# Kernel optimization log

Measured on AMD Instinct MI355X. Metric: run time of the kernel, lower is better.

## Reference

```python
import jax, jax.numpy as jnp
import numpy as np

N, T, DIN, E, D, L, G = 50000, 1, 7, 800000, 64, 3, 64


def _lin(key, fi, fo):
    k1, k2 = jax.random.split(key)
    s = 1.0 / np.sqrt(fi)
    return (jax.random.uniform(k1, (fi, fo), jnp.float32, -s, s),
            jax.random.uniform(k2, (fo,), jnp.float32, -s, s))


def setup_inputs() -> dict:
    key = jax.random.key(0)
    ks = jax.random.split(key, 16)
    x = jax.random.normal(ks[0], (N, T, DIN), jnp.float32)
    edge_index = jax.random.randint(ks[1], (2, E), 0, N).astype(jnp.int64)
    edge_attr = jax.random.uniform(ks[2], (E, T), jnp.float32)
    batch = jnp.sort(jax.random.randint(ks[3], (N,), 0, G)).astype(jnp.int64)
    degree = jax.random.uniform(ks[4], (N,), jnp.float32)
    W_en, b_en = _lin(ks[5], DIN, D)
    W_ene, b_ene = _lin(ks[6], DIN + 1, D - 1)
    W_agg, b_agg = _lin(ks[7], D, D)
    Wm = []; bm = []; Wu = []; bu = []
    for l in range(L):
        w, b = _lin(jax.random.fold_in(ks[8], l), 2 * D, D); Wm.append(w); bm.append(b)
        w, b = _lin(jax.random.fold_in(ks[9], l), 2 * D, D); Wu.append(w); bu.append(b)
    Wm = jnp.stack(Wm); bm = jnp.stack(bm); Wu = jnp.stack(Wu); bu = jnp.stack(bu)
    W_g, b_g = _lin(ks[10], D, D)
    W_r, b_r = _lin(ks[11], 2 * D, 1)
    return dict(x=x, edge_index=edge_index, edge_attr=edge_attr, batch=batch,
                degree=degree, num_graphs=G,
                W_en=W_en, b_en=b_en, W_ene=W_ene, b_ene=b_ene,
                W_agg=W_agg, b_agg=b_agg, Wm=Wm, bm=bm, Wu=Wu, bu=bu,
                W_g=W_g, b_g=b_g, W_r=W_r, b_r=b_r)


def _scatter_mean(vals, idx, n):
    # vals: [M, T, F] -> [n, T, F]; empty segments -> 0 (count clamped to 1)
    s = jax.ops.segment_sum(vals, idx, num_segments=n)
    c = jax.ops.segment_sum(jnp.ones((vals.shape[0], 1, 1), vals.dtype), idx, num_segments=n)
    return s / jnp.maximum(c, 1.0)


def reference(x, edge_index, edge_attr, batch, degree, num_graphs,
              W_en, b_en, W_ene, b_ene, W_agg, b_agg,
              Wm, bm, Wu, bu, W_g, b_g, W_r, b_r):
    relu = jax.nn.relu
    col, row = edge_index[0], edge_index[1]
    n = x.shape[0]
    x_emb = relu(x @ W_en + b_en)                                   # [N,T,D]
    # node+edge embedding: gather source nodes, append edge_attr, mean over dst
    ne_in = jnp.concatenate([x[col], edge_attr[:, :, None]], axis=-1)  # [E,T,DIN+1]
    node_edge = _scatter_mean(ne_in, row, n)                        # [N,T,DIN+1]
    node_edge = relu(node_edge @ W_ene + b_ene)                     # [N,T,D-1]
    deg_max = jax.ops.segment_max(degree, batch, num_segments=num_graphs)
    degree_norm = deg_max[batch][:, None, None]                     # [N,1,1] -> broadcast over T
    degree_norm = jnp.broadcast_to(degree_norm, (n, node_edge.shape[1], 1))
    x_agg_emb = relu(jnp.concatenate([node_edge, degree_norm], axis=-1) @ W_agg + b_agg)
    for l in range(Wm.shape[0]):
        x_agg = _scatter_mean(edge_attr[:, :, None] * x_emb[col], row, n)   # [N,T,D]
        m = relu(jnp.concatenate([x_agg, x_agg_emb], axis=-1) @ Wm[l] + bm[l])
        x_emb = relu(jnp.concatenate([x_emb, m], axis=-1) @ Wu[l] + bu[l])
    g_agg = _scatter_mean(x_emb, batch, num_graphs)                 # [G,T,D]
    g_agg = g_agg @ W_g + b_g
    inp = jnp.concatenate([g_agg[batch], x_emb], axis=-1)           # [N,T,2D]
    q = relu(inp) @ W_r + b_r                                       # [N,T,1]
    return jnp.squeeze(q, axis=-1)                                  # [N,T]
```

## Files before the change

### kernel.cpp

```cpp
#include <hip/hip_runtime.h>

constexpr int NN  = 50000;
constexpr int EE  = 800000;
constexpr int GG  = 64;
constexpr int LL  = 3;

__device__ __forceinline__ float reluf(float x) { return x > 0.f ? x : 0.f; }

__global__ void k_count(const int* __restrict__ ei, int* __restrict__ cnt,
                        int* __restrict__ rel) {
    int e = blockIdx.x * blockDim.x + threadIdx.x;
    if (e >= EE) return;
    rel[e] = atomicAdd(&cnt[ei[EE + e]], 1);
}

__global__ void k_scan1(const int* __restrict__ cnt, int* __restrict__ off,
                        int* __restrict__ bsum,
                        const int* __restrict__ batch, const float* __restrict__ degree,
                        unsigned* __restrict__ degmax_u, int* __restrict__ g_cnt) {
    __shared__ int s[256];
    __shared__ unsigned smax[GG];
    __shared__ int scnt[GG];
    int t = threadIdx.x, blk = blockIdx.x;
    if (t < GG) { smax[t] = 0u; scnt[t] = 0; }
    int base = blk * 1024 + t * 4;
    int v[4], tot = 0;
#pragma unroll
    for (int j = 0; j < 4; j++) {
        int i = base + j;
        v[j] = (i < NN) ? cnt[i] : 0;
        tot += v[j];
    }
    s[t] = tot;
    __syncthreads();
    {
        int curb = -1; unsigned cur = 0u; int ccnt = 0;
#pragma unroll
        for (int j = 0; j < 4; j++) {
            int i = base + j;
            if (i < NN) {
                int b = batch[i];
                unsigned d = __float_as_uint(degree[i]);
                if (b != curb) {
                    if (curb >= 0) { atomicMax(&smax[curb], cur); atomicAdd(&scnt[curb], ccnt); }
                    curb = b; cur = d; ccnt = 1;
                } else {
                    if (d > cur) cur = d;
                    ccnt++;
                }
            }
        }
        if (curb >= 0) { atomicMax(&smax[curb], cur); atomicAdd(&scnt[curb], ccnt); }
    }
    for (int d = 1; d < 256; d <<= 1) {
        int a = (t >= d) ? s[t - d] : 0;
        __syncthreads();
        s[t] += a;
        __syncthreads();
    }
    int run = s[t] - tot;
#pragma unroll
    for (int j = 0; j < 4; j++) {
        int i = base + j;
        if (i <= NN) off[i] = run;
        run += v[j];
    }
    if (t == 255) bsum[blk] = s[255];
    __syncthreads();
    if (t < GG) {
        if (smax[t] != 0u) atomicMax(&degmax_u[t], smax[t]);
        if (scnt[t] != 0)  atomicAdd(&g_cnt[t], scnt[t]);
    }
}
__global__ void k_scan3(int* __restrict__ off, const int* __restrict__ bsum) {
    __shared__ int sadd;
    if (threadIdx.x == 0) {
        int chunk = blockIdx.x >> 2;
        int run = 0;
        for (int b = 0; b < chunk; b++) run += bsum[b];
        sadd = run;
    }
    __syncthreads();
    int i = blockIdx.x * blockDim.x + threadIdx.x;
    if (i <= NN) off[i] += sadd;
}

__global__ void k_fill(const int* __restrict__ ei, const float* __restrict__ ea,
                       const int* __restrict__ off, const int* __restrict__ rel,
                       int2* __restrict__ sorted) {
    int e = blockIdx.x * blockDim.x + threadIdx.x;
    if (e >= EE) return;
    int col = ei[e];
    int row = ei[EE + e];
    sorted[off[row] + rel[e]] = make_int2(col, __float_as_int(ea[e]));
}

__global__ void k_nesum(const float* __restrict__ x, const int2* __restrict__ sorted,
                        const int* __restrict__ off, float* __restrict__ ne_sum) {
    int gwave = (blockIdx.x * blockDim.x + threadIdx.x) >> 6;
    int lane = threadIdx.x & 63;
    int sub = lane >> 3;
    int f = lane & 7;
    int node = gwave * 8 + sub;
    if (node >= NN) return;
    int jb = off[node], je = off[node + 1];
    float a0 = 0.f, a1 = 0.f, a2 = 0.f, a3 = 0.f;
    int j = jb;
    for (; j + 4 <= je; j += 4) {
        int2 p0 = sorted[j], p1 = sorted[j + 1], p2 = sorted[j + 2], p3 = sorted[j + 3];
        a0 += (f < 7) ? x[(size_t)p0.x * 7 + f] : __int_as_float(p0.y);
        a1 += (f < 7) ? x[(size_t)p1.x * 7 + f] : __int_as_float(p1.y);
        a2 += (f < 7) ? x[(size_t)p2.x * 7 + f] : __int_as_float(p2.y);
        a3 += (f < 7) ? x[(size_t)p3.x * 7 + f] : __int_as_float(p3.y);
    }
    for (; j < je; j++) {
        int2 p = sorted[j];
        a0 += (f < 7) ? x[(size_t)p.x * 7 + f] : __int_as_float(p.y);
    }
    ne_sum[(size_t)node * 8 + f] = (a0 + a1) + (a2 + a3);
}

__global__ __launch_bounds__(256) void k_node_pre(
        const float* __restrict__ x, const int* __restrict__ cnt,
        const float* __restrict__ ne_sum, const unsigned* __restrict__ degmax_u,
        const int* __restrict__ batch,
        const float* __restrict__ W_en, const float* __restrict__ b_en,
        const float* __restrict__ W_ene, const float* __restrict__ b_ene,
        const float* __restrict__ W_agg, const float* __restrict__ b_agg,
        float* __restrict__ x_emb, float* __restrict__ xae) {
    __shared__ float sWen[7 * 64], sben[64];
    __shared__ float sWene[8 * 63], sbene[63];
    __shared__ float srow[4][64];
    for (int i = threadIdx.x; i < 7 * 64; i += 256) sWen[i] = W_en[i];
    for (int i = threadIdx.x; i < 64; i += 256) sben[i] = b_en[i];
    for (int i = threadIdx.x; i < 8 * 63; i += 256) sWene[i] = W_ene[i];
    for (int i = threadIdx.x; i < 63; i += 256) sbene[i] = b_ene[i];
    __syncthreads();
    int lane = threadIdx.x & 63;
    int slot = threadIdx.x >> 6;
    int wave = blockIdx.x * 4 + slot;
    int nw = gridDim.x * 4;
    float wagg[64];
#pragma unroll
    for (int k = 0; k < 64; k++) wagg[k] = W_agg[(size_t)k * 64 + lane];
    float bagg = b_agg[lane];
    for (int i = wave; i < NN; i += nw) {
        float acc = sben[lane];
#pragma unroll
        for (int k = 0; k < 7; k++) acc += x[(size_t)i * 7 + k] * sWen[k * 64 + lane];
        x_emb[(size_t)i * 64 + lane] = reluf(acc);
        float c = (float)cnt[i]; if (c < 1.f) c = 1.f;
        float rc = 1.f / c;
        int oo = lane < 63 ? lane : 0;
        float4 n0 = *(const float4*)(ne_sum + (size_t)i * 8);
        float4 n1 = *(const float4*)(ne_sum + (size_t)i * 8 + 4);
        float na = sbene[oo];
        na += (n0.x * rc) * sWene[0 * 63 + oo];
        na += (n0.y * rc) * sWene[1 * 63 + oo];
        na += (n0.z * rc) * sWene[2 * 63 + oo];
        na += (n0.w * rc) * sWene[3 * 63 + oo];
        na += (n1.x * rc) * sWene[4 * 63 + oo];
        na += (n1.y * rc) * sWene[5 * 63 + oo];
        na += (n1.z * rc) * sWene[6 * 63 + oo];
        na += (n1.w * rc) * sWene[7 * 63 + oo];
        na = reluf(na);
        float dn = __uint_as_float(degmax_u[batch[i]]);
        float val = (lane < 63) ? na : dn;
        srow[slot][lane] = val;
        const float* rp = &srow[slot][0];
        float a0 = bagg, a1 = 0.f;
#pragma unroll
        for (int kb = 0; kb < 64; kb += 8) {
            float4 x0 = *(const float4*)(rp + kb);
            float4 x1 = *(const float4*)(rp + kb + 4);
            a0 = fmaf(x0.x, wagg[kb + 0], a0); a1 = fmaf(x0.y, wagg[kb + 1], a1);
            a0 = fmaf(x0.z, wagg[kb + 2], a0); a1 = fmaf(x0.w, wagg[kb + 3], a1);
            a0 = fmaf(x1.x, wagg[kb + 4], a0); a1 = fmaf(x1.y, wagg[kb + 5], a1);
            a0 = fmaf(x1.z, wagg[kb + 6], a0); a1 = fmaf(x1.w, wagg[kb + 7], a1);
        }
        xae[(size_t)i * 64 + lane] = reluf(a0 + a1);
    }
}

template <int GSUM>
__global__ __launch_bounds__(256, 3) void k_mv128(
        const float* __restrict__ inA, const float* __restrict__ inB,
        const float* __restrict__ W, const float* __restrict__ b,
        float* __restrict__ out, int nwaves,
        const int* __restrict__ batch, float* __restrict__ g_sum) {
    __shared__ float sbuf[4][2][128];
    int slot = threadIdx.x >> 6;
    int gwave = (blockIdx.x * blockDim.x + threadIdx.x) >> 6;
    int lane = threadIdx.x & 63;
    int per = (NN + nwaves - 1) / nwaves;
    int n0 = gwave * per;
    int n1 = n0 + per; if (n1 > NN) n1 = NN;
    if (n0 >= n1) return;
    float w[128];
#pragma unroll
    for (int k = 0; k < 128; k++) w[k] = W[(size_t)k * 64 + lane];
    float bias = b[lane];
    sbuf[slot][0][lane]      = inA[(size_t)n0 * 64 + lane];
    sbuf[slot][0][64 + lane] = inB[(size_t)n0 * 64 + lane];
    int cntn = n1 - n0;
    float gacc = 0.f;
    int curb = GSUM ? batch[n0] : 0;
    for (int i = 0; i < cntn; i++) {
        int n = n0 + i;
        float vA = 0.f, vB = 0.f;
        if (i + 1 < cntn) {
            vA = inA[(size_t)(n + 1) * 64 + lane];
            vB = inB[(size_t)(n + 1) * 64 + lane];
        }
        const float* bufp = &sbuf[slot][i & 1][0];
        float a0 = 0.f, a1 = 0.f;
#pragma unroll
        for (int kb = 0; kb < 128; kb += 8) {
            float4 x0 = *(const float4*)(bufp + kb);
            float4 x1 = *(const float4*)(bufp + kb + 4);
            a0 = fmaf(x0.x, w[kb + 0], a0); a1 = fmaf(x0.y, w[kb + 1], a1);
            a0 = fmaf(x0.z, w[kb + 2], a0); a1 = fmaf(x0.w, w[kb + 3], a1);
            a0 = fmaf(x1.x, w[kb + 4], a0); a1 = fmaf(x1.y, w[kb + 5], a1);
            a0 = fmaf(x1.z, w[kb + 6], a0); a1 = fmaf(x1.w, w[kb + 7], a1);
        }
        float r = reluf(a0 + a1 + bias);
        out[(size_t)n * 64 + lane] = r;
        if (GSUM) {
            int bb = batch[n];
            if (bb != curb) {
                unsafeAtomicAdd(&g_sum[curb * 64 + lane], gacc);
                gacc = 0.f; curb = bb;
            }
            gacc += r;
        }
        if (i + 1 < cntn) {
            sbuf[slot][(i + 1) & 1][lane]      = vA;
            sbuf[slot][(i + 1) & 1][64 + lane] = vB;
        }
    }
    if (GSUM) unsafeAtomicAdd(&g_sum[curb * 64 + lane], gacc);
}

__global__ __launch_bounds__(256) void k_layer_agg(
        const float* __restrict__ xemb, const int* __restrict__ off,
        const int* __restrict__ cnt, const int2* __restrict__ sorted,
        float* __restrict__ xagg) {
    int lane = threadIdx.x & 63;
    int slot = threadIdx.x >> 6;
    int wave = blockIdx.x * 4 + slot;
    int nw = gridDim.x * 4;
    for (int i = wave; i < NN; i += nw) {
        int jb = off[i], je = off[i + 1];
        float a0 = 0.f, a1 = 0.f, a2 = 0.f, a3 = 0.f;
        float a4 = 0.f, a5 = 0.f, a6 = 0.f, a7 = 0.f;
        int j = jb;
        for (; j + 8 <= je; j += 8) {
            int2 p0 = sorted[j + 0], p1 = sorted[j + 1];
            int2 p2 = sorted[j + 2], p3 = sorted[j + 3];
            int2 p4 = sorted[j + 4], p5 = sorted[j + 5];
            int2 p6 = sorted[j + 6], p7 = sorted[j + 7];
            a0 = fmaf(__int_as_float(p0.y), xemb[(size_t)p0.x * 64 + lane], a0);
            a1 = fmaf(__int_as_float(p1.y), xemb[(size_t)p1.x * 64 + lane], a1);
            a2 = fmaf(__int_as_float(p2.y), xemb[(size_t)p2.x * 64 + lane], a2);
            a3 = fmaf(__int_as_float(p3.y), xemb[(size_t)p3.x * 64 + lane], a3);
            a4 = fmaf(__int_as_float(p4.y), xemb[(size_t)p4.x * 64 + lane], a4);
            a5 = fmaf(__int_as_float(p5.y), xemb[(size_t)p5.x * 64 + lane], a5);
            a6 = fmaf(__int_as_float(p6.y), xemb[(size_t)p6.x * 64 + lane], a6);
            a7 = fmaf(__int_as_float(p7.y), xemb[(size_t)p7.x * 64 + lane], a7);
        }
        if (j < je) {
            int jl = je - 1;
            int2 p0 = sorted[j + 0];
            int2 p1 = sorted[min(j + 1, jl)];
            int2 p2 = sorted[min(j + 2, jl)];
            int2 p3 = sorted[min(j + 3, jl)];
            int2 p4 = sorted[min(j + 4, jl)];
            int2 p5 = sorted[min(j + 5, jl)];
            int2 p6 = sorted[min(j + 6, jl)];
            int2 p7 = sorted[min(j + 7, jl)];
            float s0 = __int_as_float(p0.y);
            float s1 = (j + 1 < je) ? __int_as_float(p1.y) : 0.f;
            float s2 = (j + 2 < je) ? __int_as_float(p2.y) : 0.f;
            float s3 = (j + 3 < je) ? __int_as_float(p3.y) : 0.f;
            float s4 = (j + 4 < je) ? __int_as_float(p4.y) : 0.f;
            float s5 = (j + 5 < je) ? __int_as_float(p5.y) : 0.f;
            float s6 = (j + 6 < je) ? __int_as_float(p6.y) : 0.f;
            float s7 = (j + 7 < je) ? __int_as_float(p7.y) : 0.f;
            a0 = fmaf(s0, xemb[(size_t)p0.x * 64 + lane], a0);
            a1 = fmaf(s1, xemb[(size_t)p1.x * 64 + lane], a1);
            a2 = fmaf(s2, xemb[(size_t)p2.x * 64 + lane], a2);
            a3 = fmaf(s3, xemb[(size_t)p3.x * 64 + lane], a3);
            a4 = fmaf(s4, xemb[(size_t)p4.x * 64 + lane], a4);
            a5 = fmaf(s5, xemb[(size_t)p5.x * 64 + lane], a5);
            a6 = fmaf(s6, xemb[(size_t)p6.x * 64 + lane], a6);
            a7 = fmaf(s7, xemb[(size_t)p7.x * 64 + lane], a7);
        }
        float acc = ((a0 + a1) + (a2 + a3)) + ((a4 + a5) + (a6 + a7));
        float c = (float)cnt[i]; if (c < 1.f) c = 1.f;
        xagg[(size_t)i * 64 + lane] = acc * (1.f / c);
    }
}

__global__ void k_graph_emb(const float* __restrict__ g_sum, const int* __restrict__ g_cnt,
                            const float* __restrict__ W_g, const float* __restrict__ b_g,
                            float* __restrict__ g_agg) {
    __shared__ float sin[4 * 64];
    int lane = threadIdx.x & 63;
    int slot = threadIdx.x >> 6;
    int g = blockIdx.x * 4 + slot;
    if (g >= GG) return;
    float c = (float)g_cnt[g]; if (c < 1.f) c = 1.f;
    sin[slot * 64 + lane] = g_sum[g * 64 + lane] * (1.f / c);
    __syncthreads();
    float acc = b_g[lane];
    for (int k = 0; k < 64; k++) acc += sin[slot * 64 + k] * W_g[k * 64 + lane];
    g_agg[g * 64 + lane] = acc;
}

__global__ void k_readout(const float* __restrict__ g_agg, const float* __restrict__ xemb,
                          const int* __restrict__ batch,
                          const float* __restrict__ W_r, const float* __restrict__ b_r,
                          float* __restrict__ out) {
    int i = blockIdx.x * blockDim.x + threadIdx.x;
    if (i >= NN) return;
    int b = batch[i];
    float acc = b_r[0];
    const float* ga = g_agg + (size_t)b * 64;
    const float* xe = xemb + (size_t)i * 64;
#pragma unroll 8
    for (int k = 0; k < 64; k++) acc += reluf(ga[k]) * W_r[k];
#pragma unroll 8
    for (int k = 0; k < 64; k++) acc += reluf(xe[k]) * W_r[64 + k];
    out[i] = acc;
}

extern "C" void kernel_launch(void* const* d_in, const int* in_sizes, int n_in,
                              void* d_out, int out_size, void* d_ws, size_t ws_size,
                              hipStream_t stream) {
    const float* x      = (const float*)d_in[0];
    const int*   ei     = (const int*)d_in[1];
    const float* ea     = (const float*)d_in[2];
    const int*   batch  = (const int*)d_in[3];
    const float* degree = (const float*)d_in[4];
    const float* W_en  = (const float*)d_in[6];
    const float* b_en  = (const float*)d_in[7];
    const float* W_ene = (const float*)d_in[8];
    const float* b_ene = (const float*)d_in[9];
    const float* W_agg = (const float*)d_in[10];
    const float* b_agg = (const float*)d_in[11];
    const float* Wm    = (const float*)d_in[12];
    const float* bm    = (const float*)d_in[13];
    const float* Wu    = (const float*)d_in[14];
    const float* bu    = (const float*)d_in[15];
    const float* W_g   = (const float*)d_in[16];
    const float* b_g   = (const float*)d_in[17];
    const float* W_r   = (const float*)d_in[18];
    const float* b_r   = (const float*)d_in[19];
    float* out = (float*)d_out;

    char* ws = (char*)d_ws;
    size_t o = 0;
    int*      cnt      = (int*)(ws + o * 4);      o += NN;
    unsigned* degmax_u = (unsigned*)(ws + o * 4); o += GG;
    float*    g_sum    = (float*)(ws + o * 4);    o += GG * 64;
    int*      g_cnt    = (int*)(ws + o * 4);      o += GG;
    size_t zero_bytes = o * 4;
    int*      off      = (int*)(ws + o * 4);      o += NN + 1;
    int*      bsum     = (int*)(ws + o * 4);      o += 64;
    int*      rel      = (int*)(ws + o * 4);      o += EE;
    float*    ne_sum   = (float*)(ws + o * 4);    o += (size_t)NN * 8;
    o = (o + 1) & ~(size_t)1;
    int2*     sorted   = (int2*)(ws + o * 4);     o += (size_t)EE * 2;
    float*    xae      = (float*)(ws + o * 4);    o += (size_t)NN * 64;
    float*    xA       = (float*)(ws + o * 4);    o += (size_t)NN * 64;
    float*    xB       = (float*)(ws + o * 4);    o += (size_t)NN * 64;
    float*    xagg     = (float*)(ws + o * 4);    o += (size_t)NN * 64;
    float*    mbuf     = (float*)(ws + o * 4);    o += (size_t)NN * 64;
    float*    g_agg    = (float*)(ws + o * 4);    o += GG * 64;

    hipMemsetAsync(d_ws, 0, zero_bytes, stream);

    const int NB_SCAN = 49;
    const int MV_BLOCKS = 768;
    const int MV_WAVES = MV_BLOCKS * 4;
    k_count<<<(EE + 255) / 256, 256, 0, stream>>>(ei, cnt, rel);
    k_scan1<<<NB_SCAN, 256, 0, stream>>>(cnt, off, bsum, batch, degree, degmax_u, g_cnt);
    k_scan3<<<(NN + 256) / 256, 256, 0, stream>>>(off, bsum);
    k_fill<<<(EE + 255) / 256, 256, 0, stream>>>(ei, ea, off, rel, sorted);
    k_nesum<<<((NN + 7) / 8 * 64 + 255) / 256, 256, 0, stream>>>(x, sorted, off, ne_sum);
    k_node_pre<<<1024, 256, 0, stream>>>(x, cnt, ne_sum, degmax_u, batch,
                                         W_en, b_en, W_ene, b_ene, W_agg, b_agg,
                                         xA, xae);
    const float* cur = xA;
    float* nxt = xB;
    for (int l = 0; l < LL; l++) {
        const float* WmL = Wm + (size_t)l * 128 * 64;
        const float* WuL = Wu + (size_t)l * 128 * 64;
        k_layer_agg<<<2048, 256, 0, stream>>>(cur, off, cnt, sorted, xagg);
        k_mv128<0><<<MV_BLOCKS, 256, 0, stream>>>(xagg, xae, WmL, bm + l * 64,
                                                  mbuf, MV_WAVES, nullptr, nullptr);
        if (l < LL - 1) {
            k_mv128<0><<<MV_BLOCKS, 256, 0, stream>>>(cur, mbuf, WuL, bu + l * 64,
                                                      nxt, MV_WAVES, nullptr, nullptr);
        } else {
            k_mv128<1><<<MV_BLOCKS, 256, 0, stream>>>(cur, mbuf, WuL, bu + l * 64,
                                                      nxt, MV_WAVES, batch, g_sum);
        }
        float* t = (float*)cur; cur = nxt; nxt = t;
    }
    k_graph_emb<<<16, 256, 0, stream>>>(g_sum, g_cnt, W_g, b_g, g_agg);
    k_readout<<<(NN + 255) / 256, 256, 0, stream>>>(g_agg, cur, batch, W_r, b_r, out);
}
```

Baseline: 442.7 us.

## Drop rel buffer, use one wave per node in aggregation, precompute graph readout dot

The CSR fill no longer reads a stored per-edge rank. It now takes a second atomic counter at fill time, which removes a 3.2MB write and read. The layer aggregation switches from a persistent grid-stride loop over 2048 blocks to one wave per node, with a grid sized to cover every node. The graph readout half is collapsed into one scalar per graph, computed in k_graph_emb with a wave shuffle reduction, so k_readout no longer does 64 extra MACs per node. The cost is that edge order within each CSR segment becomes nondeterministic, and it also adds more block launches for aggregation.

```diff
diff --git a/kernel.cpp b/kernel.cpp
--- a/kernel.cpp
+++ b/kernel.cpp
@@ -7,11 +7,10 @@
 
 __device__ __forceinline__ float reluf(float x) { return x > 0.f ? x : 0.f; }
 
-__global__ void k_count(const int* __restrict__ ei, int* __restrict__ cnt,
-                        int* __restrict__ rel) {
+__global__ void k_count(const int* __restrict__ ei, int* __restrict__ cnt) {
     int e = blockIdx.x * blockDim.x + threadIdx.x;
     if (e >= EE) return;
-    rel[e] = atomicAdd(&cnt[ei[EE + e]], 1);
+    atomicAdd(&cnt[ei[EE + e]], 1);
 }
 
 __global__ void k_scan1(const int* __restrict__ cnt, int* __restrict__ off,
@@ -86,13 +85,14 @@
 }
 
 __global__ void k_fill(const int* __restrict__ ei, const float* __restrict__ ea,
-                       const int* __restrict__ off, const int* __restrict__ rel,
+                       const int* __restrict__ off, int* __restrict__ cnt2,
                        int2* __restrict__ sorted) {
     int e = blockIdx.x * blockDim.x + threadIdx.x;
     if (e >= EE) return;
     int col = ei[e];
     int row = ei[EE + e];
-    sorted[off[row] + rel[e]] = make_int2(col, __float_as_int(ea[e]));
+    int r = atomicAdd(&cnt2[row], 1);
+    sorted[off[row] + r] = make_int2(col, __float_as_int(ea[e]));
 }
 
 __global__ void k_nesum(const float* __restrict__ x, const int2* __restrict__ sorted,
@@ -246,10 +246,9 @@
         const int* __restrict__ cnt, const int2* __restrict__ sorted,
         float* __restrict__ xagg) {
     int lane = threadIdx.x & 63;
-    int slot = threadIdx.x >> 6;
-    int wave = blockIdx.x * 4 + slot;
-    int nw = gridDim.x * 4;
-    for (int i = wave; i < NN; i += nw) {
+    int i = (blockIdx.x * blockDim.x + threadIdx.x) >> 6;
+    if (i >= NN) return;
+    {
         int jb = off[i], je = off[i + 1];
         float a0 = 0.f, a1 = 0.f, a2 = 0.f, a3 = 0.f;
         float a4 = 0.f, a5 = 0.f, a6 = 0.f, a7 = 0.f;
@@ -303,7 +302,7 @@
 
 __global__ void k_graph_emb(const float* __restrict__ g_sum, const int* __restrict__ g_cnt,
                             const float* __restrict__ W_g, const float* __restrict__ b_g,
-                            float* __restrict__ g_agg) {
+                            const float* __restrict__ W_r, float* __restrict__ dotA) {
     __shared__ float sin[4 * 64];
     int lane = threadIdx.x & 63;
     int slot = threadIdx.x >> 6;
@@ -314,21 +313,21 @@
     __syncthreads();
     float acc = b_g[lane];
     for (int k = 0; k < 64; k++) acc += sin[slot * 64 + k] * W_g[k * 64 + lane];
-    g_agg[g * 64 + lane] = acc;
-}
-
-__global__ void k_readout(const float* __restrict__ g_agg, const float* __restrict__ xemb,
+    float v = reluf(acc) * W_r[lane];
+#pragma unroll
+    for (int d = 1; d < 64; d <<= 1) v += __shfl_xor(v, d, 64);
+    if (lane == 0) dotA[g] = v;
+}
+
+__global__ void k_readout(const float* __restrict__ dotA, const float* __restrict__ xemb,
                           const int* __restrict__ batch,
                           const float* __restrict__ W_r, const float* __restrict__ b_r,
                           float* __restrict__ out) {
     int i = blockIdx.x * blockDim.x + threadIdx.x;
     if (i >= NN) return;
     int b = batch[i];
-    float acc = b_r[0];
-    const float* ga = g_agg + (size_t)b * 64;
+    float acc = b_r[0] + dotA[b];
     const float* xe = xemb + (size_t)i * 64;
-#pragma unroll 8
-    for (int k = 0; k < 64; k++) acc += reluf(ga[k]) * W_r[k];
 #pragma unroll 8
     for (int k = 0; k < 64; k++) acc += reluf(xe[k]) * W_r[64 + k];
     out[i] = acc;
@@ -361,13 +360,13 @@
     char* ws = (char*)d_ws;
     size_t o = 0;
     int*      cnt      = (int*)(ws + o * 4);      o += NN;
+    int*      cnt2     = (int*)(ws + o * 4);      o += NN;
     unsigned* degmax_u = (unsigned*)(ws + o * 4); o += GG;
     float*    g_sum    = (float*)(ws + o * 4);    o += GG * 64;
     int*      g_cnt    = (int*)(ws + o * 4);      o += GG;
     size_t zero_bytes = o * 4;
     int*      off      = (int*)(ws + o * 4);      o += NN + 1;
     int*      bsum     = (int*)(ws + o * 4);      o += 64;
-    int*      rel      = (int*)(ws + o * 4);      o += EE;
     float*    ne_sum   = (float*)(ws + o * 4);    o += (size_t)NN * 8;
     o = (o + 1) & ~(size_t)1;
     int2*     sorted   = (int2*)(ws + o * 4);     o += (size_t)EE * 2;
@@ -376,27 +375,28 @@
     float*    xB       = (float*)(ws + o * 4);    o += (size_t)NN * 64;
     float*    xagg     = (float*)(ws + o * 4);    o += (size_t)NN * 64;
     float*    mbuf     = (float*)(ws + o * 4);    o += (size_t)NN * 64;
-    float*    g_agg    = (float*)(ws + o * 4);    o += GG * 64;
+    float*    dotA     = (float*)(ws + o * 4);    o += GG;
 
     hipMemsetAsync(d_ws, 0, zero_bytes, stream);
 
     const int NB_SCAN = 49;
     const int MV_BLOCKS = 768;
     const int MV_WAVES = MV_BLOCKS * 4;
-    k_count<<<(EE + 255) / 256, 256, 0, stream>>>(ei, cnt, rel);
+    k_count<<<(EE + 255) / 256, 256, 0, stream>>>(ei, cnt);
     k_scan1<<<NB_SCAN, 256, 0, stream>>>(cnt, off, bsum, batch, degree, degmax_u, g_cnt);
     k_scan3<<<(NN + 256) / 256, 256, 0, stream>>>(off, bsum);
-    k_fill<<<(EE + 255) / 256, 256, 0, stream>>>(ei, ea, off, rel, sorted);
+    k_fill<<<(EE + 255) / 256, 256, 0, stream>>>(ei, ea, off, cnt2, sorted);
     k_nesum<<<((NN + 7) / 8 * 64 + 255) / 256, 256, 0, stream>>>(x, sorted, off, ne_sum);
     k_node_pre<<<1024, 256, 0, stream>>>(x, cnt, ne_sum, degmax_u, batch,
                                          W_en, b_en, W_ene, b_ene, W_agg, b_agg,
                                          xA, xae);
     const float* cur = xA;
     float* nxt = xB;
+    const int AGG_BLOCKS = (NN * 64 + 255) / 256;
     for (int l = 0; l < LL; l++) {
         const float* WmL = Wm + (size_t)l * 128 * 64;
         const float* WuL = Wu + (size_t)l * 128 * 64;
-        k_layer_agg<<<2048, 256, 0, stream>>>(cur, off, cnt, sorted, xagg);
+        k_layer_agg<<<AGG_BLOCKS, 256, 0, stream>>>(cur, off, cnt, sorted, xagg);
         k_mv128<0><<<MV_BLOCKS, 256, 0, stream>>>(xagg, xae, WmL, bm + l * 64,
                                                   mbuf, MV_WAVES, nullptr, nullptr);
         if (l < LL - 1) {
@@ -408,6 +408,6 @@
         }
         float* t = (float*)cur; cur = nxt; nxt = t;
     }
-    k_graph_emb<<<16, 256, 0, stream>>>(g_sum, g_cnt, W_g, b_g, g_agg);
-    k_readout<<<(NN + 255) / 256, 256, 0, stream>>>(g_agg, cur, batch, W_r, b_r, out);
-}
+    k_graph_emb<<<16, 256, 0, stream>>>(g_sum, g_cnt, W_g, b_g, W_r, dotA);
+    k_readout<<<(NN + 255) / 256, 256, 0, stream>>>(dotA, cur, batch, W_r, b_r, out);
+}
```

Result: slower. 461.1 us (+4.2%).
